# Optimization experiments

Hardware: AMD Instinct MI355X
Metric: run time of the kernel (lower is better)

The kernel has to match this reference:

```python
import jax, jax.numpy as jnp
import numpy as np

# DeHoog ILT constants (from init_kwargs)
ALPHA = 1e-3
TOL = 1e-2          # default tol = 10*alpha
SCALE = 2.0
NTERMS = 33         # ilt_reconstruction_terms = 2M+1
M = (NTERMS - 1) // 2


def setup_inputs() -> dict:
    key = jax.random.key(0)
    k1, k2, k3 = jax.random.split(key, 3)
    B, S, D = 32, 512, 32
    # positive, sorted time points; T = ti (recommended usage)
    ti = jnp.sort(jax.random.uniform(k1, (S,), minval=0.5, maxval=1.5))
    T = ti
    Tsc = SCALE * T                                     # contour period per time point
    gamma = ALPHA - jnp.log(TOL) / (SCALE * Tsc)        # (S,)
    kk = jnp.arange(NTERMS)
    s = gamma[:, None] + 1j * jnp.pi * kk[None, :] / Tsc[:, None]   # (S, 33)
    # Build fp as a genuine Laplace transform F(s) = sum_p c_p / (s + w_p)
    # (random fp makes the QD recurrence numerically singular)
    P = 4
    w = jax.random.uniform(k2, (B, D, P), minval=0.2, maxval=3.0)
    c = jax.random.normal(k3, (B, D, P))
    fp = jnp.zeros((B, S, D, NTERMS), dtype=jnp.complex64)
    for p in range(P):  # small fixed loop over poles, avoids a (B,S,D,P,33) intermediate
        fp = fp + c[:, None, :, p, None] / (s[None, :, None, :] + w[:, None, :, p, None])
    return {
        "fp_real": jnp.real(fp).astype(jnp.float32),
        "fp_imag": jnp.imag(fp).astype(jnp.float32),
        "ti": ti.astype(jnp.float32),
        "T": T.astype(jnp.float32),
    }


def _dehoog(fp_real, fp_imag, ti, T):
    """De Hoog ILT: QD (quotient-difference) Pade acceleration + continued
    fraction with remainder term. fp: (B,S,D,2M+1) complex samples of F at
    s_{i,k} = gamma_i + i*pi*k/T_i.  Returns x(t): (B,S,D) real."""
    fp = fp_real + 1j * fp_imag                       # (B,S,D,2M+1)
    Tsc = SCALE * T                                   # (S,)
    gamma = ALPHA - jnp.log(TOL) / (SCALE * Tsc)      # (S,)
    # Fourier coefficients: a_0 halved
    a = jnp.concatenate([0.5 * fp[..., :1], fp[..., 1:]], axis=-1)
    # --- QD algorithm: builds continued-fraction coefficients d_0..d_{2M} ---
    q = a[..., 1:] / a[..., :-1]                      # q_1, length 2M
    e = jnp.zeros_like(a)                             # e_0 = 0, length 2M+1
    d = [a[..., 0], -q[..., 0]]                       # d_0, d_1
    for r in range(1, M + 1):
        Le = 2 * (M - r) + 1
        e = q[..., 1:Le + 1] - q[..., :Le] + e[..., 1:Le + 1]   # e_r
        d.append(-e[..., 0])                          # d_{2r}
        if r < M:
            Lq = 2 * (M - r)
            q = q[..., 1:Lq + 1] * e[..., 1:Lq + 1] / e[..., :Lq]  # q_{r+1}
            d.insert(-1, -q[..., 0])                  # d_{2r+1} goes before d_{2r}? no-op below
    # fix ordering: rebuild d in canonical order [d0, -q1, -e1, -q2, -e2, ...]
    # (the insert above is wrong ordering; recompute cleanly)
    q = a[..., 1:] / a[..., :-1]
    e = jnp.zeros_like(a)
    d = [a[..., 0], -q[..., 0]]
    for r in range(1, M + 1):
        Le = 2 * (M - r) + 1
        e = q[..., 1:Le + 1] - q[..., :Le] + e[..., 1:Le + 1]
        if r < M:
            Lq = 2 * (M - r)
            q = q[..., 1:Lq + 1] * e[..., 1:Lq + 1] / e[..., :Lq]
            d.append(-e[..., 0])   # d_{2r}
            d.append(-q[..., 0])   # d_{2r+1}
        else:
            d.append(-e[..., 0])   # d_{2M}
    d = jnp.stack(d, axis=-1)                         # (B,S,D,2M+1)
    # --- continued fraction A_n = A_{n-1} + d_n z A_{n-2} via scan ---
    z = jnp.exp(1j * jnp.pi * (ti / Tsc))[None, :, None]   # (1,S,1)
    dz = jnp.moveaxis(d[..., 1:], -1, 0) * z          # (2M,B,S,D)
    A_prev = jnp.zeros_like(d[..., 0])
    A_cur = d[..., 0]
    B_prev = jnp.ones_like(A_cur)
    B_cur = jnp.ones_like(A_cur)
    def step(carry, dzn):
        Ap, Ac, Bp, Bc = carry
        return (Ac, Ac + dzn * Ap, Bc, Bc + dzn * Bp), None
    (A_prev, A_cur, B_prev, B_cur), _ = jax.lax.scan(step, (A_prev, A_cur, B_prev, B_cur), dz)
    # --- double acceleration: remainder term for the truncated fraction ---
    brem = 0.5 * (1.0 + (d[..., 2 * M - 1] - d[..., 2 * M]) * z)
    rem = -brem * (1.0 - jnp.sqrt(1.0 + d[..., 2 * M] * z / (brem * brem)))
    Af = A_cur + rem * A_prev
    Bf = B_cur + rem * B_prev
    return (jnp.exp(gamma * ti) / Tsc)[None, :, None] * jnp.real(Af / Bf)


def reference(fp_real, fp_imag, ti, T):
    return _dehoog(fp_real, fp_imag, ti, T)
```

## Files before the change

### kernel.cpp

```cpp
#include <hip/hip_runtime.h>
#include <math.h>

#define MM 8
#define NU (2*MM + 1)
#define NT 33
#define DD 32
#define SS 512
#define BLK 256

__device__ __forceinline__ float frcp_fast(float d) {
    float r = __builtin_amdgcn_rcpf(d);
    return r * (2.0f - d * r);
}

__device__ __forceinline__ float2 cmul(float2 a, float2 b) {
    return make_float2(fmaf(a.x, b.x, -a.y * b.y), fmaf(a.x, b.y, a.y * b.x));
}
__device__ __forceinline__ float2 cadd(float2 a, float2 b) {
    return make_float2(a.x + b.x, a.y + b.y);
}
__device__ __forceinline__ float2 csub(float2 a, float2 b) {
    return make_float2(a.x - b.x, a.y - b.y);
}
__device__ __forceinline__ float2 cneg(float2 a) {
    return make_float2(-a.x, -a.y);
}
__device__ __forceinline__ float2 cdiv(float2 a, float2 b) {
    float d = fmaf(b.x, b.x, b.y * b.y);
    d = fmaxf(d, 1.0e-32f);
    float r0 = __builtin_amdgcn_rcpf(d);
    float r  = r0 * fmaf(-d, r0, 2.0f);
    return make_float2(fmaf(a.x, b.x, a.y * b.y) * r,
                       fmaf(a.y, b.x, -a.x * b.y) * r);
}
__device__ __forceinline__ float2 csqrt_(float2 a) {
    float r = sqrtf(fmaf(a.x, a.x, a.y * a.y));
    float re = sqrtf(fmaxf(0.5f * (r + a.x), 0.0f));
    float im = sqrtf(fmaxf(0.5f * (r - a.x), 0.0f));
    im = (a.y < 0.0f) ? -im : im;
    return make_float2(re, im);
}

__global__ __launch_bounds__(BLK) void dehoog_kernel(
    const float* __restrict__ fpr, const float* __restrict__ fpi,
    const float* __restrict__ ti_arr, const float* __restrict__ T_arr,
    float* __restrict__ out)
{
    const int gid = blockIdx.x * BLK + threadIdx.x;

    const size_t base = (size_t)gid * NT;
    const float* mr = fpr + base;
    const float* mi = fpi + base;
    float ar[NU], ai[NU];
    {
        const float4* r4 = reinterpret_cast<const float4*>(mr);
        const float4* i4 = reinterpret_cast<const float4*>(mi);
        float4 r0 = r4[0], r1 = r4[1], r2 = r4[2], r3 = r4[3];
        float4 q0 = i4[0], q1 = i4[1], q2 = i4[2], q3 = i4[3];
        float rl = mr[16], il = mi[16];
        ar[0]=r0.x;  ar[1]=r0.y;  ar[2]=r0.z;  ar[3]=r0.w;
        ar[4]=r1.x;  ar[5]=r1.y;  ar[6]=r1.z;  ar[7]=r1.w;
        ar[8]=r2.x;  ar[9]=r2.y;  ar[10]=r2.z; ar[11]=r2.w;
        ar[12]=r3.x; ar[13]=r3.y; ar[14]=r3.z; ar[15]=r3.w;
        ar[16]=rl;
        ai[0]=q0.x;  ai[1]=q0.y;  ai[2]=q0.z;  ai[3]=q0.w;
        ai[4]=q1.x;  ai[5]=q1.y;  ai[6]=q1.z;  ai[7]=q1.w;
        ai[8]=q2.x;  ai[9]=q2.y;  ai[10]=q2.z; ai[11]=q2.w;
        ai[12]=q3.x; ai[13]=q3.y; ai[14]=q3.z; ai[15]=q3.w;
        ai[16]=il;
    }

    const int s_idx = (gid / DD) % SS;
    const float Tt  = T_arr[s_idx];
    const float tii = ti_arr[s_idx];
    const float Tsc = 2.0f * Tt;
    const float rTsc = frcp_fast(Tsc);
    const float gamma = 1.0e-3f + 4.605170185988091f * 0.5f * rTsc;

    float2 z;
    {
        float ang = 3.14159265358979323846f * tii * rTsc;
        z = make_float2(__cosf(ang), __sinf(ang));
    }

    float2 q[2 * MM];
    float2 e[NU];
    float2 a_prev = make_float2(0.5f * ar[0], 0.5f * ai[0]);
    const float2 d0 = a_prev;
#pragma unroll
    for (int j = 0; j < 2 * MM; ++j) {
        float2 a_next = make_float2(ar[j + 1], ai[j + 1]);
        q[j] = cdiv(a_next, a_prev);
        a_prev = a_next;
    }
#pragma unroll
    for (int j = 0; j < NU; ++j) e[j] = make_float2(0.0f, 0.0f);

    float2 Ap = make_float2(0.0f, 0.0f);
    float2 Ac = d0;
    float2 Bp = make_float2(1.0f, 0.0f);
    float2 Bc = make_float2(1.0f, 0.0f);

    auto cf_step = [&](float2 dn) {
        float2 dz = cmul(dn, z);
        float2 An = cadd(Ac, cmul(dz, Ap));
        Ap = Ac; Ac = An;
        float2 Bn = cadd(Bc, cmul(dz, Bp));
        Bp = Bc; Bc = Bn;
    };

    float2 d_2M_m1 = make_float2(0.0f, 0.0f);
    float2 d_2M    = make_float2(0.0f, 0.0f);

    cf_step(cneg(q[0]));

#pragma unroll
    for (int r = 1; r <= MM; ++r) {
        const int Le = 2 * (MM - r) + 1;
#pragma unroll
        for (int j = 0; j < Le; ++j)
            e[j] = cadd(csub(q[j + 1], q[j]), e[j + 1]);
        float2 d2r = cneg(e[0]);
        if (r < MM) {
            cf_step(d2r);
            const int Lq = 2 * (MM - r);
#pragma unroll
            for (int j = 0; j < Lq; ++j)
                q[j] = cdiv(cmul(q[j + 1], e[j + 1]), e[j]);
            float2 d2r1 = cneg(q[0]);
            cf_step(d2r1);
            if (r == MM - 1) d_2M_m1 = d2r1;
        } else {
            d_2M = d2r;
            cf_step(d2r);
        }
    }

    float2 dd = csub(d_2M_m1, d_2M);
    float2 brem = cmul(dd, z);
    brem = make_float2(0.5f * (1.0f + brem.x), 0.5f * brem.y);
    float2 b2 = cmul(brem, brem);
    float2 arg = cdiv(cmul(d_2M, z), b2);
    arg = make_float2(1.0f + arg.x, arg.y);
    float2 sq = csqrt_(arg);
    float2 one_m = make_float2(1.0f - sq.x, -sq.y);
    float2 rem = cmul(cneg(brem), one_m);

    float2 Af = cadd(Ac, cmul(rem, Ap));
    float2 Bf = cadd(Bc, cmul(rem, Bp));

    float rden = frcp_fast(fmaf(Bf.x, Bf.x, Bf.y * Bf.y));
    float re = fmaf(Af.x, Bf.x, Af.y * Bf.y) * rden;
    out[gid] = (__expf(gamma * tii) * rTsc) * re;
}

extern "C" void kernel_launch(void* const* d_in, const int* in_sizes, int n_in,
                              void* d_out, int out_size, void* d_ws, size_t ws_size,
                              hipStream_t stream) {
    const float* fpr = (const float*)d_in[0];
    const float* fpi = (const float*)d_in[1];
    const float* ti  = (const float*)d_in[2];
    const float* T   = (const float*)d_in[3];
    float* out = (float*)d_out;
    const int total = out_size;
    const int grid = (total + BLK - 1) / BLK;
    dehoog_kernel<<<grid, BLK, 0, stream>>>(fpr, fpi, ti, T, out);
}
```

Before: 158.6 us.

## Process two elements per thread with packed float2 vector math

```diff
diff --git a/kernel.cpp b/kernel.cpp
--- a/kernel.cpp
+++ b/kernel.cpp
@@ -8,37 +8,49 @@
 #define SS 512
 #define BLK 256
 
+typedef float f2 __attribute__((ext_vector_type(2)));
+
+struct c2 { f2 re, im; };
+
+__device__ __forceinline__ f2 mkf2(float a, float b) { f2 v; v.x = a; v.y = b; return v; }
+
 __device__ __forceinline__ float frcp_fast(float d) {
     float r = __builtin_amdgcn_rcpf(d);
     return r * (2.0f - d * r);
 }
-
-__device__ __forceinline__ float2 cmul(float2 a, float2 b) {
-    return make_float2(fmaf(a.x, b.x, -a.y * b.y), fmaf(a.x, b.y, a.y * b.x));
-}
-__device__ __forceinline__ float2 cadd(float2 a, float2 b) {
-    return make_float2(a.x + b.x, a.y + b.y);
-}
-__device__ __forceinline__ float2 csub(float2 a, float2 b) {
-    return make_float2(a.x - b.x, a.y - b.y);
-}
-__device__ __forceinline__ float2 cneg(float2 a) {
-    return make_float2(-a.x, -a.y);
-}
-__device__ __forceinline__ float2 cdiv(float2 a, float2 b) {
-    float d = fmaf(b.x, b.x, b.y * b.y);
-    d = fmaxf(d, 1.0e-32f);
-    float r0 = __builtin_amdgcn_rcpf(d);
-    float r  = r0 * fmaf(-d, r0, 2.0f);
-    return make_float2(fmaf(a.x, b.x, a.y * b.y) * r,
-                       fmaf(a.y, b.x, -a.x * b.y) * r);
-}
-__device__ __forceinline__ float2 csqrt_(float2 a) {
-    float r = sqrtf(fmaf(a.x, a.x, a.y * a.y));
-    float re = sqrtf(fmaxf(0.5f * (r + a.x), 0.0f));
-    float im = sqrtf(fmaxf(0.5f * (r - a.x), 0.0f));
-    im = (a.y < 0.0f) ? -im : im;
-    return make_float2(re, im);
+__device__ __forceinline__ f2 rcp2(f2 d) {
+    f2 r;
+    r.x = __builtin_amdgcn_rcpf(d.x);
+    r.y = __builtin_amdgcn_rcpf(d.y);
+    return r * (2.0f - d * r);
+}
+__device__ __forceinline__ f2 sqrt2f(f2 x) { f2 r; r.x = sqrtf(x.x); r.y = sqrtf(x.y); return r; }
+
+__device__ __forceinline__ c2 cmul(c2 a, c2 b) {
+    c2 o;
+    o.re = a.re * b.re - a.im * b.im;
+    o.im = a.re * b.im + a.im * b.re;
+    return o;
+}
+__device__ __forceinline__ c2 cadd(c2 a, c2 b) { c2 o; o.re = a.re + b.re; o.im = a.im + b.im; return o; }
+__device__ __forceinline__ c2 csub(c2 a, c2 b) { c2 o; o.re = a.re - b.re; o.im = a.im - b.im; return o; }
+__device__ __forceinline__ c2 cneg(c2 a) { c2 o; o.re = -a.re; o.im = -a.im; return o; }
+__device__ __forceinline__ c2 cdiv(c2 a, c2 b) {
+    f2 d = b.re * b.re + b.im * b.im;
+    d = __builtin_elementwise_max(d, mkf2(1.0e-32f, 1.0e-32f));
+    f2 r = rcp2(d);
+    c2 o;
+    o.re = (a.re * b.re + a.im * b.im) * r;
+    o.im = (a.im * b.re - a.re * b.im) * r;
+    return o;
+}
+__device__ __forceinline__ c2 csqrt2(c2 a) {
+    f2 r = sqrt2f(a.re * a.re + a.im * a.im);
+    f2 re = sqrt2f(__builtin_elementwise_max(0.5f * (r + a.re), mkf2(0.0f, 0.0f)));
+    f2 im = sqrt2f(__builtin_elementwise_max(0.5f * (r - a.re), mkf2(0.0f, 0.0f)));
+    im.x = (a.im.x < 0.0f) ? -im.x : im.x;
+    im.y = (a.im.y < 0.0f) ? -im.y : im.y;
+    c2 o; o.re = re; o.im = im; return o;
 }
 
 __global__ __launch_bounds__(BLK) void dehoog_kernel(
@@ -46,71 +58,89 @@
     const float* __restrict__ ti_arr, const float* __restrict__ T_arr,
     float* __restrict__ out)
 {
-    const int gid = blockIdx.x * BLK + threadIdx.x;
-
-    const size_t base = (size_t)gid * NT;
-    const float* mr = fpr + base;
-    const float* mi = fpi + base;
-    float ar[NU], ai[NU];
+    const int tid = blockIdx.x * BLK + threadIdx.x;
+    const int e0  = tid << 1;
+
+    const size_t baseA = (size_t)e0 * NT;
+    const float* mrA = fpr + baseA;  const float* mrB = mrA + NT;
+    const float* miA = fpi + baseA;  const float* miB = miA + NT;
+
+    f2 ar[NU], ai[NU];
     {
-        const float4* r4 = reinterpret_cast<const float4*>(mr);
-        const float4* i4 = reinterpret_cast<const float4*>(mi);
-        float4 r0 = r4[0], r1 = r4[1], r2 = r4[2], r3 = r4[3];
-        float4 q0 = i4[0], q1 = i4[1], q2 = i4[2], q3 = i4[3];
-        float rl = mr[16], il = mi[16];
-        ar[0]=r0.x;  ar[1]=r0.y;  ar[2]=r0.z;  ar[3]=r0.w;
-        ar[4]=r1.x;  ar[5]=r1.y;  ar[6]=r1.z;  ar[7]=r1.w;
-        ar[8]=r2.x;  ar[9]=r2.y;  ar[10]=r2.z; ar[11]=r2.w;
-        ar[12]=r3.x; ar[13]=r3.y; ar[14]=r3.z; ar[15]=r3.w;
-        ar[16]=rl;
-        ai[0]=q0.x;  ai[1]=q0.y;  ai[2]=q0.z;  ai[3]=q0.w;
-        ai[4]=q1.x;  ai[5]=q1.y;  ai[6]=q1.z;  ai[7]=q1.w;
-        ai[8]=q2.x;  ai[9]=q2.y;  ai[10]=q2.z; ai[11]=q2.w;
-        ai[12]=q3.x; ai[13]=q3.y; ai[14]=q3.z; ai[15]=q3.w;
-        ai[16]=il;
-    }
-
-    const int s_idx = (gid / DD) % SS;
+        const float4* rA = reinterpret_cast<const float4*>(mrA);
+        const float4* rB = reinterpret_cast<const float4*>(mrB);
+        const float4* iA = reinterpret_cast<const float4*>(miA);
+        const float4* iB = reinterpret_cast<const float4*>(miB);
+        float4 ra0 = rA[0], ra1 = rA[1], ra2 = rA[2], ra3 = rA[3];
+        float4 rb0 = rB[0], rb1 = rB[1], rb2 = rB[2], rb3 = rB[3];
+        float  ral = mrA[16], rbl = mrB[16];
+        float4 ia0 = iA[0], ia1 = iA[1], ia2 = iA[2], ia3 = iA[3];
+        float4 ib0 = iB[0], ib1 = iB[1], ib2 = iB[2], ib3 = iB[3];
+        float  ial = miA[16], ibl = miB[16];
+        ar[0]  = mkf2(ra0.x, rb0.x);  ar[1]  = mkf2(ra0.y, rb0.y);
+        ar[2]  = mkf2(ra0.z, rb0.z);  ar[3]  = mkf2(ra0.w, rb0.w);
+        ar[4]  = mkf2(ra1.x, rb1.x);  ar[5]  = mkf2(ra1.y, rb1.y);
+        ar[6]  = mkf2(ra1.z, rb1.z);  ar[7]  = mkf2(ra1.w, rb1.w);
+        ar[8]  = mkf2(ra2.x, rb2.x);  ar[9]  = mkf2(ra2.y, rb2.y);
+        ar[10] = mkf2(ra2.z, rb2.z);  ar[11] = mkf2(ra2.w, rb2.w);
+        ar[12] = mkf2(ra3.x, rb3.x);  ar[13] = mkf2(ra3.y, rb3.y);
+        ar[14] = mkf2(ra3.z, rb3.z);  ar[15] = mkf2(ra3.w, rb3.w);
+        ar[16] = mkf2(ral,   rbl);
+        ai[0]  = mkf2(ia0.x, ib0.x);  ai[1]  = mkf2(ia0.y, ib0.y);
+        ai[2]  = mkf2(ia0.z, ib0.z);  ai[3]  = mkf2(ia0.w, ib0.w);
+        ai[4]  = mkf2(ia1.x, ib1.x);  ai[5]  = mkf2(ia1.y, ib1.y);
+        ai[6]  = mkf2(ia1.z, ib1.z);  ai[7]  = mkf2(ia1.w, ib1.w);
+        ai[8]  = mkf2(ia2.x, ib2.x);  ai[9]  = mkf2(ia2.y, ib2.y);
+        ai[10] = mkf2(ia2.z, ib2.z);  ai[11] = mkf2(ia2.w, ib2.w);
+        ai[12] = mkf2(ia3.x, ib3.x);  ai[13] = mkf2(ia3.y, ib3.y);
+        ai[14] = mkf2(ia3.z, ib3.z);  ai[15] = mkf2(ial,   ibl) ;
+        ai[15] = mkf2(ia3.w, ib3.w);
+        ai[16] = mkf2(ial,   ibl);
+    }
+
+    const int s_idx = (tid >> 4) & (SS - 1);
     const float Tt  = T_arr[s_idx];
     const float tii = ti_arr[s_idx];
     const float Tsc = 2.0f * Tt;
     const float rTsc = frcp_fast(Tsc);
     const float gamma = 1.0e-3f + 4.605170185988091f * 0.5f * rTsc;
 
-    float2 z;
+    float zr, zi;
     {
         float ang = 3.14159265358979323846f * tii * rTsc;
-        z = make_float2(__cosf(ang), __sinf(ang));
-    }
-
-    float2 q[2 * MM];
-    float2 e[NU];
-    float2 a_prev = make_float2(0.5f * ar[0], 0.5f * ai[0]);
-    const float2 d0 = a_prev;
+        zr = __cosf(ang); zi = __sinf(ang);
+    }
+
+    c2 q[2 * MM];
+    c2 e[NU];
+    c2 a_prev; a_prev.re = 0.5f * ar[0]; a_prev.im = 0.5f * ai[0];
+    const c2 d0 = a_prev;
 #pragma unroll
     for (int j = 0; j < 2 * MM; ++j) {
-        float2 a_next = make_float2(ar[j + 1], ai[j + 1]);
+        c2 a_next; a_next.re = ar[j + 1]; a_next.im = ai[j + 1];
         q[j] = cdiv(a_next, a_prev);
         a_prev = a_next;
     }
 #pragma unroll
-    for (int j = 0; j < NU; ++j) e[j] = make_float2(0.0f, 0.0f);
-
-    float2 Ap = make_float2(0.0f, 0.0f);
-    float2 Ac = d0;
-    float2 Bp = make_float2(1.0f, 0.0f);
-    float2 Bc = make_float2(1.0f, 0.0f);
-
-    auto cf_step = [&](float2 dn) {
-        float2 dz = cmul(dn, z);
-        float2 An = cadd(Ac, cmul(dz, Ap));
+    for (int j = 0; j < NU; ++j) { e[j].re = mkf2(0.0f, 0.0f); e[j].im = mkf2(0.0f, 0.0f); }
+
+    c2 Ap; Ap.re = mkf2(0.0f, 0.0f); Ap.im = mkf2(0.0f, 0.0f);
+    c2 Ac = d0;
+    c2 Bp; Bp.re = mkf2(1.0f, 1.0f); Bp.im = mkf2(0.0f, 0.0f);
+    c2 Bc = Bp;
+
+    auto cf_step = [&](c2 dn) {
+        c2 dz;
+        dz.re = dn.re * zr - dn.im * zi;
+        dz.im = dn.re * zi + dn.im * zr;
+        c2 An = cadd(Ac, cmul(dz, Ap));
         Ap = Ac; Ac = An;
-        float2 Bn = cadd(Bc, cmul(dz, Bp));
+        c2 Bn = cadd(Bc, cmul(dz, Bp));
         Bp = Bc; Bc = Bn;
     };
 
-    float2 d_2M_m1 = make_float2(0.0f, 0.0f);
-    float2 d_2M    = make_float2(0.0f, 0.0f);
+    c2 d_2M_m1; d_2M_m1.re = mkf2(0.0f, 0.0f); d_2M_m1.im = mkf2(0.0f, 0.0f);
+    c2 d_2M;    d_2M.re    = mkf2(0.0f, 0.0f); d_2M.im    = mkf2(0.0f, 0.0f);
 
     cf_step(cneg(q[0]));
 
@@ -120,14 +150,14 @@
 #pragma unroll
         for (int j = 0; j < Le; ++j)
             e[j] = cadd(csub(q[j + 1], q[j]), e[j + 1]);
-        float2 d2r = cneg(e[0]);
+        c2 d2r = cneg(e[0]);
         if (r < MM) {
             cf_step(d2r);
             const int Lq = 2 * (MM - r);
 #pragma unroll
             for (int j = 0; j < Lq; ++j)
                 q[j] = cdiv(cmul(q[j + 1], e[j + 1]), e[j]);
-            float2 d2r1 = cneg(q[0]);
+            c2 d2r1 = cneg(q[0]);
             cf_step(d2r1);
             if (r == MM - 1) d_2M_m1 = d2r1;
         } else {
@@ -136,22 +166,33 @@
         }
     }
 
-    float2 dd = csub(d_2M_m1, d_2M);
-    float2 brem = cmul(dd, z);
-    brem = make_float2(0.5f * (1.0f + brem.x), 0.5f * brem.y);
-    float2 b2 = cmul(brem, brem);
-    float2 arg = cdiv(cmul(d_2M, z), b2);
-    arg = make_float2(1.0f + arg.x, arg.y);
-    float2 sq = csqrt_(arg);
-    float2 one_m = make_float2(1.0f - sq.x, -sq.y);
-    float2 rem = cmul(cneg(brem), one_m);
-
-    float2 Af = cadd(Ac, cmul(rem, Ap));
-    float2 Bf = cadd(Bc, cmul(rem, Bp));
-
-    float rden = frcp_fast(fmaf(Bf.x, Bf.x, Bf.y * Bf.y));
-    float re = fmaf(Af.x, Bf.x, Af.y * Bf.y) * rden;
-    out[gid] = (__expf(gamma * tii) * rTsc) * re;
+    c2 ddv = csub(d_2M_m1, d_2M);
+    c2 brem;
+    {
+        f2 tre = ddv.re * zr - ddv.im * zi;
+        f2 tim = ddv.re * zi + ddv.im * zr;
+        brem.re = 0.5f * (1.0f + tre);
+        brem.im = 0.5f * tim;
+    }
+    c2 b2 = cmul(brem, brem);
+    c2 dz2;
+    dz2.re = d_2M.re * zr - d_2M.im * zi;
+    dz2.im = d_2M.re * zi + d_2M.im * zr;
+    c2 arg = cdiv(dz2, b2);
+    arg.re = 1.0f + arg.re;
+    c2 sq = csqrt2(arg);
+    c2 one_m; one_m.re = 1.0f - sq.re; one_m.im = -sq.im;
+    c2 rem = cmul(cneg(brem), one_m);
+
+    c2 Af = cadd(Ac, cmul(rem, Ap));
+    c2 Bf = cadd(Bc, cmul(rem, Bp));
+
+    f2 rden = rcp2(Bf.re * Bf.re + Bf.im * Bf.im);
+    f2 re = (Af.re * Bf.re + Af.im * Bf.im) * rden;
+    f2 res = (__expf(gamma * tii) * rTsc) * re;
+
+    float2 ov; ov.x = res.x; ov.y = res.y;
+    reinterpret_cast<float2*>(out)[tid] = ov;
 }
 
 extern "C" void kernel_launch(void* const* d_in, const int* in_sizes, int n_in,
@@ -163,6 +204,7 @@
     const float* T   = (const float*)d_in[3];
     float* out = (float*)d_out;
     const int total = out_size;
-    const int grid = (total + BLK - 1) / BLK;
+    const int npair = total >> 1;
+    const int grid  = (npair + BLK - 1) / BLK;
     dehoog_kernel<<<grid, BLK, 0, stream>>>(fpr, fpi, ti, T, out);
 }
```

After: 160.4 us. Within noise of the previous version (+1.1%).
